# Kernel optimization log

Hardware: AMD Instinct MI355X
Metric: run time of the kernel (lower is better)

Reference implementation:

```python
import jax, jax.numpy as jnp
import numpy as np

N, E = 50000, 400000
N_INP, H, D = 256, 4, 32
HID = H * D
TN, TE, L, N_OUT = 4, 6, 2, 16
SQRT_D = float(np.sqrt(D))


def setup_inputs() -> dict:
    key = jax.random.key(0)
    ks = jax.random.split(key, 16)
    s = 0.05
    return {
        "x": jax.random.normal(ks[0], (N, N_INP), jnp.float32),
        "adapt_W": jax.random.normal(ks[1], (TN, N_INP, HID), jnp.float32) * s,
        "adapt_b": jnp.zeros((TN, HID), jnp.float32),
        "Wk": jax.random.normal(ks[2], (L, TN, HID, HID), jnp.float32) * s,
        "Wq": jax.random.normal(ks[3], (L, TN, HID, HID), jnp.float32) * s,
        "Wv": jax.random.normal(ks[4], (L, TN, HID, HID), jnp.float32) * s,
        "pri": jnp.ones((L, H, TE), jnp.float32),
        "Wa": jax.random.normal(ks[5], (L, H, TE, D, D), jnp.float32) * s,
        "Wm": jax.random.normal(ks[6], (L, H, TE, D, D), jnp.float32) * s,
        "Wla": jax.random.normal(ks[7], (L, TN, HID, HID), jnp.float32) * s,
        "skip": jnp.ones((L, TN), jnp.float32),
        "gamma": jnp.ones((L, HID), jnp.float32),
        "beta": jnp.zeros((L, HID), jnp.float32),
        "out_W": jax.random.normal(ks[8], (HID, N_OUT), jnp.float32) * s,
        "out_b": jnp.zeros((N_OUT,), jnp.float32),
        "ntype": jax.random.randint(ks[9], (N,), 0, TN),
        "etype": jax.random.randint(ks[10], (E,), 0, TE),
        "src": jax.random.randint(ks[11], (E,), 0, N),
        "dst": jax.random.randint(ks[12], (E,), 0, N),
    }


def typed_linear(x, W, types):
    # out[i] = x[i] @ W[types[i]]  (TypedLinear / per-type nn.Linear loop)
    out = jnp.zeros((x.shape[0], W.shape[-1]), x.dtype)
    for t in range(W.shape[0]):
        out = jnp.where((types == t)[:, None], x @ W[t], out)
    return out


def hgt_layer(h, ntype, etype, src, dst, Wk, Wq, Wv, pri, Wa, Wm, Wla, skip, gamma, beta):
    k = typed_linear(h, Wk, ntype).reshape(N, H, D)
    q = typed_linear(h, Wq, ntype).reshape(N, H, D)
    v = typed_linear(h, Wv, ntype).reshape(N, H, D)
    k_e, q_e, v_e = k[src], q[dst], v[src]  # [E,H,D] gathers
    a = jnp.zeros((E, H), h.dtype)
    m = jnp.zeros((E, H, D), h.dtype)
    for t in range(TE):  # small fixed loop over edge types (relation matrices)
        sel = etype == t
        kw = jnp.einsum('ehd,hdo->eho', k_e, Wa[:, t])
        sc = (kw * q_e).sum(-1) * pri[:, t][None, :] / SQRT_D  # [E,H]
        a = jnp.where(sel[:, None], sc, a)
        mt = jnp.einsum('ehd,hdo->eho', v_e, Wm[:, t])
        m = jnp.where(sel[:, None, None], mt, m)
    # edge softmax over incoming edges of each destination node
    amax = jax.ops.segment_max(a, dst, num_segments=N)
    ex = jnp.exp(a - amax[dst])
    den = jax.ops.segment_sum(ex, dst, num_segments=N)
    attn = ex / den[dst]
    agg = jax.ops.segment_sum(m * attn[:, :, None], dst, num_segments=N).reshape(N, HID)
    ha = typed_linear(agg, Wla, ntype)
    alpha = jax.nn.sigmoid(skip)[ntype][:, None]
    out = ha * alpha + h * (1.0 - alpha)
    mu = out.mean(-1, keepdims=True)
    var = jnp.mean((out - mu) ** 2, -1, keepdims=True)
    return (out - mu) / jnp.sqrt(var + 1e-5) * gamma + beta


def forward(x, adapt_W, adapt_b, Wk, Wq, Wv, pri, Wa, Wm, Wla, skip, gamma, beta, out_W, out_b, ntype, etype, src, dst):
    # per-node-type adapt linear + exact GELU
    h = typed_linear(x, adapt_W, ntype) + adapt_b[ntype]
    h = jax.nn.gelu(h, approximate=False)
    for l in range(L):
        h = hgt_layer(h, ntype, etype, src, dst, Wk[l], Wq[l], Wv[l], pri[l], Wa[l], Wm[l], Wla[l], skip[l], gamma[l], beta[l])
    return h @ out_W + out_b


def reference(x, adapt_W, adapt_b, Wk, Wq, Wv, pri, Wa, Wm, Wla, skip, gamma, beta, out_W, out_b, ntype, etype, src, dst):
    return forward(x, adapt_W, adapt_b, Wk, Wq, Wv, pri, Wa, Wm, Wla, skip, gamma, beta, out_W, out_b, ntype, etype, src, dst)
```

## Files before the change

### kernel.cpp

```cpp
#include <hip/hip_runtime.h>
#include <hip/hip_bf16.h>
#include <math.h>

#define NN   50000
#define EE   400000
#define NINP 256
#define HH   4
#define DD   32
#define HIDD 128
#define TNN  4
#define TEE  6
#define LLL  2
#define NOUTT 16
#define NB   196


typedef __attribute__((ext_vector_type(8))) short bf16x8;
typedef __attribute__((ext_vector_type(4))) float f32x4;

__device__ __forceinline__ float bf_lo(unsigned u) { return __uint_as_float(u << 16); }
__device__ __forceinline__ float bf_hi(unsigned u) { return __uint_as_float(u & 0xFFFF0000u); }
__device__ __forceinline__ unsigned f2bf(float f) {
    unsigned u = __float_as_uint(f);
    u += 0x7FFFu + ((u >> 16) & 1u);
    return (u >> 16);
}

__global__ void k_init(int* __restrict__ deg, int* __restrict__ cur, int* __restrict__ ncnt,
                       int* __restrict__ ncur, int* __restrict__ nperm) {
    int i = blockIdx.x * 256 + threadIdx.x;
    if (i < NN) { deg[i] = 0; cur[i] = 0; }
    if (i < 16) { ncnt[i] = 0; ncur[i] = 0; }
    if (i < NN + 512) nperm[i] = -1;
}

__global__ void k_count_edges(const int* __restrict__ dst, int* __restrict__ deg) {
    int e = blockIdx.x * 256 + threadIdx.x;
    if (e < EE) atomicAdd(&deg[dst[e]], 1);
}
__global__ void k_count_types(const int* __restrict__ ntype, int* __restrict__ ncnt) {
    int n = blockIdx.x * 256 + threadIdx.x;
    int lane = threadIdx.x & 63;
    int t = (n < NN) ? ntype[n] : -1;
#pragma unroll
    for (int tt = 0; tt < TNN; tt++) {
        unsigned long long mask = __ballot(t == tt);
        if (mask && lane == (__ffsll((unsigned long long)mask) - 1))
            atomicAdd(&ncnt[tt], __popcll(mask));
    }
}
__global__ void k_scan1(const int* __restrict__ deg, int* __restrict__ bsum) {
    int i = blockIdx.x * 256 + threadIdx.x;
    int lane = threadIdx.x & 63, wv = threadIdx.x >> 6;
    __shared__ int ws[4];
    int x = (i < NN) ? deg[i] : 0;
#pragma unroll
    for (int off = 1; off < 64; off <<= 1) x += __shfl_xor(x, off);
    if (lane == 0) ws[wv] = x;
    __syncthreads();
    if (threadIdx.x == 0) bsum[blockIdx.x] = ws[0] + ws[1] + ws[2] + ws[3];
}
__global__ void k_scan2(const int* __restrict__ bsum, int* __restrict__ bpre,
                        const int* __restrict__ ncnt, int* __restrict__ meta) {
    __shared__ int ws[4];
    int tid = threadIdx.x, lane = tid & 63, wv = tid >> 6;
    int v = (tid < NB) ? bsum[tid] : 0;
    int x = v;
#pragma unroll
    for (int off = 1; off < 64; off <<= 1) {
        int y = __shfl_up(x, off);
        if (lane >= off) x += y;
    }
    if (lane == 63) ws[wv] = x;
    __syncthreads();
    if (tid == 0) { int a = 0; for (int w = 0; w < 4; w++) { int s = ws[w]; ws[w] = a; a += s; } }
    __syncthreads();
    if (tid < NB) bpre[tid] = x - v + ws[wv];
    if (tid == 0) {
        int acc = 0;
        meta[0] = 0;
        for (int t = 0; t < TNN; t++) { acc += ((ncnt[t] + 63) >> 6) << 6; meta[t + 1] = acc; }
    }
}
__global__ void k_scan3(const int* __restrict__ deg, const int* __restrict__ bpre,
                        int* __restrict__ offs) {
    int b = blockIdx.x;
    int tid = threadIdx.x, lane = tid & 63, wv = tid >> 6;
    int i = b * 256 + tid;
    __shared__ int ws[4];
    int v = (i < NN) ? deg[i] : 0;
    int x = v;
#pragma unroll
    for (int off = 1; off < 64; off <<= 1) {
        int y = __shfl_up(x, off);
        if (lane >= off) x += y;
    }
    if (lane == 63) ws[wv] = x;
    __syncthreads();
    if (tid == 0) { int a = 0; for (int w = 0; w < 4; w++) { int s = ws[w]; ws[w] = a; a += s; } }
    __syncthreads();
    if (i < NN) offs[i + 1] = x + ws[wv] + bpre[b];
    if (b == 0 && tid == 0) offs[0] = 0;
}
__global__ void k_scatter_edges(const int* __restrict__ dst, const int* __restrict__ offs,
                                int* __restrict__ cur, int* __restrict__ eidx) {
    int e = blockIdx.x * 256 + threadIdx.x;
    if (e < EE) {
        int d = dst[e];
        int p = atomicAdd(&cur[d], 1);
        eidx[offs[d] + p] = e;
    }
}
__global__ void k_scatter_nodes(const int* __restrict__ ntype, const int* __restrict__ meta,
                                int* __restrict__ ncur, int* __restrict__ nperm) {
    int n = blockIdx.x * 256 + threadIdx.x;
    int lane = threadIdx.x & 63;
    int t = (n < NN) ? ntype[n] : -1;
#pragma unroll
    for (int tt = 0; tt < TNN; tt++) {
        unsigned long long mask = __ballot(t == tt);
        if (t == tt) {
            int rank = __popcll(mask & ((1ull << lane) - 1ull));
            int leader = __ffsll((unsigned long long)mask) - 1;
            int b = 0;
            if (rank == 0) b = atomicAdd(&ncur[tt], __popcll(mask));
            b = __shfl(b, leader);
            nperm[meta[tt] + b + rank] = n;
        }
    }
}

__global__ void k_wt(const float* __restrict__ adapt_W, const float* __restrict__ Wk,
                     const float* __restrict__ Wla, unsigned short* __restrict__ adaptT,
                     unsigned short* __restrict__ Wf, unsigned short* __restrict__ WlaT) {
    __shared__ float Ts[64][68];
    int b = blockIdx.x, tid = threadIdx.x;
    const float* src;
    unsigned short* dst;
    int K, kt, nt;
    if (b < 32) {
        int t = b >> 3, tile = b & 7;
        K = 256; kt = tile >> 1; nt = tile & 1;
        src = adapt_W + (size_t)t * 256 * 128;
        dst = adaptT + (size_t)t * 128 * 256;
    } else if (b < 64) {
        int b2 = b - 32, l = b2 >> 4, r = b2 & 15, t = r >> 2, tile = r & 3;
        K = 128; kt = tile >> 1; nt = tile & 1;
        src = Wk + (size_t)(l * 4 + t) * 16384;
        dst = Wf + (size_t)(l * TNN + t) * 1664 * 128;
    } else {
        int b2 = b - 64, l = b2 >> 4, r = b2 & 15, t = r >> 2, tile = r & 3;
        K = 128; kt = tile >> 1; nt = tile & 1;
        src = Wla + (size_t)(l * 4 + t) * 16384;
        dst = WlaT + (size_t)(l * 4 + t) * 16384;
    }
    int k0 = kt * 64, n0 = nt * 64;
#pragma unroll
    for (int it = 0; it < 4; it++) {
        int idx = tid + it * 256;
        int row = idx >> 4, c4 = (idx & 15) * 4;
        *(float4*)(&Ts[row][c4]) = *(const float4*)(src + (size_t)(k0 + row) * 128 + n0 + c4);
    }
    __syncthreads();
#pragma unroll
    for (int it = 0; it < 2; it++) {
        int idx = tid + it * 256;
        int nn = idx >> 3, sg = (idx & 7) * 8;
        uint4 pk;
        pk.x = f2bf(Ts[sg + 0][nn]) | (f2bf(Ts[sg + 1][nn]) << 16);
        pk.y = f2bf(Ts[sg + 2][nn]) | (f2bf(Ts[sg + 3][nn]) << 16);
        pk.z = f2bf(Ts[sg + 4][nn]) | (f2bf(Ts[sg + 5][nn]) << 16);
        pk.w = f2bf(Ts[sg + 6][nn]) | (f2bf(Ts[sg + 7][nn]) << 16);
        *(uint4*)(dst + (size_t)(n0 + nn) * K + k0 + sg) = pk;
    }
}

__global__ void k_comb(const float* __restrict__ Wq, const float* __restrict__ Wa,
                       const float* __restrict__ Wv, const float* __restrict__ Wm,
                       const float* __restrict__ pri, unsigned short* __restrict__ Wf) {
    __shared__ float Ls[128][36];
    __shared__ float Ss[32][36];
    __shared__ unsigned short Ot[32][136];
    int b = blockIdx.x, tid = threadIdx.x;
    int mode = b / 192;
    int rem = b % 192;
    int l = rem / 96;
    int rem2 = rem % 96;
    int t = rem2 / 24;
    int ht = rem2 % 24;
    int hh = ht / 6, te = ht % 6;
    const float* L = (mode == 0 ? Wq : Wv) + ((size_t)(l * TNN + t)) * 16384;
    const float* S = (mode == 0 ? Wa : Wm) + ((size_t)((l * HH + hh) * TEE + te)) * 1024;
    float ps = (mode == 0) ? pri[(l * HH + hh) * TEE + te] * 0.17677669529663687f : 1.0f;
#pragma unroll
    for (int it = 0; it < 4; it++) {
        int idx = tid + it * 256;
        int kk = idx >> 3, c4 = (idx & 7) * 4;
        *(float4*)(&Ls[kk][c4]) = *(const float4*)(L + (size_t)kk * 128 + hh * 32 + c4);
    }
    {
        int r = tid >> 3, c4 = (tid & 7) * 4;
        *(float4*)(&Ss[r][c4]) = *(const float4*)(S + r * 32 + c4);
    }
    __syncthreads();
    int k = tid >> 1, half = tid & 1;
#pragma unroll
    for (int jj = 0; jj < 16; jj++) {
        int j = half * 16 + jj;
        float s = 0.f;
        if (mode == 0) {
#pragma unroll
            for (int o = 0; o < 32; o++) s += Ls[k][o] * Ss[j][o];
        } else {
#pragma unroll
            for (int d = 0; d < 32; d++) s += Ls[k][d] * Ss[d][j];
        }
        Ot[j][k] = (unsigned short)f2bf(s * ps);
    }
    __syncthreads();
    unsigned short* dst = Wf + ((size_t)(l * TNN + t) * 1664 + (mode == 0 ? 128 : 896)) * 128;
#pragma unroll
    for (int it = 0; it < 2; it++) {
        int idx = tid + it * 256;
        int j = idx >> 4, sg = (idx & 15) * 8;
        uint4 pk = *(const uint4*)(&Ot[j][sg]);
        int jg = (hh * 6 + te) * 32 + j;
        *(uint4*)(dst + (size_t)jg * 128 + sg) = pk;
    }
}

template <int K, int NCB, int EPI, int OMODE, int AF32>
__launch_bounds__(256) __global__
void k_gemm(const void* __restrict__ Av, const unsigned short* __restrict__ WT,
            const float* __restrict__ bias, float* __restrict__ Yf,
            unsigned short* __restrict__ Yb, const int* __restrict__ nperm,
            const int* __restrict__ meta, const float* __restrict__ skipv,
            const float* __restrict__ gamma, const float* __restrict__ beta,
            float* __restrict__ hres, unsigned short* __restrict__ hbout) {
    __shared__ __align__(16) char smem[52224];
    unsigned short* Ab = (unsigned short*)smem;
    unsigned short* Bs = (unsigned short*)(smem + 17408);
    float* Cb = (float*)(smem + 17408);
    const int WIDTH = NCB * 128;
    int row0 = blockIdx.x * 64;
    if (row0 >= meta[4]) return;
    int t = 0;
    while (t < 3 && row0 >= meta[t + 1]) t++;
    const unsigned short* WTt = WT + (size_t)t * WIDTH * K;
    int tid = threadIdx.x;
    int lane = tid & 63, w = tid >> 6;
    int m = lane & 15, q = lane >> 4;

#pragma unroll 1
    for (int cb = 0; cb < NCB; cb++) {
        f32x4 acc[8];
#pragma unroll
        for (int g = 0; g < 8; g++) acc[g] = (f32x4){0.f, 0.f, 0.f, 0.f};
#pragma unroll
        for (int kc = 0; kc < K / 128; kc++) {
            __syncthreads();
            if (NCB == 1 || cb == 0) {
                if (AF32) {
                    const float* A = (const float*)Av;
#pragma unroll
                    for (int it = 0; it < 8; it++) {
                        int idx = tid + it * 256;
                        int r = idx >> 5, c4 = (idx & 31) * 4;
                        int node = nperm[row0 + r];
                        float4 v = make_float4(0.f, 0.f, 0.f, 0.f);
                        if (node >= 0)
                            v = *(const float4*)(A + (size_t)node * K + kc * 128 + c4);
                        uint2 pk;
                        pk.x = f2bf(v.x) | (f2bf(v.y) << 16);
                        pk.y = f2bf(v.z) | (f2bf(v.w) << 16);
                        *(uint2*)(Ab + r * 136 + c4) = pk;
                    }
                } else {
                    const unsigned short* A = (const unsigned short*)Av;
#pragma unroll
                    for (int it = 0; it < 4; it++) {
                        int idx = tid + it * 256;
                        int r = idx >> 4, sg = idx & 15;
                        int node = nperm[row0 + r];
                        uint4 v = make_uint4(0, 0, 0, 0);
                        if (node >= 0)
                            v = *(const uint4*)(A + (size_t)node * K + kc * 128 + sg * 8);
                        *(uint4*)(Ab + r * 136 + sg * 8) = v;
                    }
                }
            }
#pragma unroll
            for (int it = 0; it < 8; it++) {
                int idx = tid + it * 256;
                int n = idx >> 4, sg = idx & 15;
                *(uint4*)(Bs + n * 136 + sg * 8) =
                    *(const uint4*)(WTt + (size_t)(cb * 128 + n) * K + kc * 128 + sg * 8);
            }
            __syncthreads();
#pragma unroll
            for (int k0 = 0; k0 < 128; k0 += 32) {
                bf16x8 a = *(const bf16x8*)(Ab + (w * 16 + m) * 136 + k0 + q * 8);
#pragma unroll
                for (int g = 0; g < 8; g++) {
                    bf16x8 bb = *(const bf16x8*)(Bs + (g * 16 + m) * 136 + k0 + q * 8);
                    acc[g] = __builtin_amdgcn_mfma_f32_16x16x32_bf16(a, bb, acc[g], 0, 0, 0);
                }
            }
        }
        __syncthreads();
#pragma unroll
        for (int g = 0; g < 8; g++)
#pragma unroll
            for (int r = 0; r < 4; r++)
                Cb[(w * 16 + q * 4 + r) * 132 + g * 16 + m] = acc[g][r];
        __syncthreads();
        if (EPI == 2) {
            float alpha = 1.0f / (1.0f + __expf(-skipv[t]));
            int off = lane * 2;
            float2 g2 = *(const float2*)(gamma + off);
            float2 b2 = *(const float2*)(beta + off);
#pragma unroll 1
            for (int it = 0; it < 16; it++) {
                int row = w * 16 + it;
                int node = nperm[row0 + row];
                if (node < 0) continue;
                float ax = Cb[row * 132 + off];
                float ay = Cb[row * 132 + off + 1];
                float2 h2 = *(const float2*)(hres + (size_t)node * 128 + off);
                float ox = ax * alpha + h2.x * (1.f - alpha);
                float oy = ay * alpha + h2.y * (1.f - alpha);
                float s = ox + oy;
#pragma unroll
                for (int mm = 1; mm < 64; mm <<= 1) s += __shfl_xor(s, mm);
                float mu = s * (1.0f / 128.0f);
                float dx = ox - mu, dy = oy - mu;
                float v2 = dx * dx + dy * dy;
#pragma unroll
                for (int mm = 1; mm < 64; mm <<= 1) v2 += __shfl_xor(v2, mm);
                float rs = rsqrtf(v2 * (1.0f / 128.0f) + 1e-5f);
                float vx = dx * rs * g2.x + b2.x;
                float vy = dy * rs * g2.y + b2.y;
                *(float2*)(hres + (size_t)node * 128 + off) = make_float2(vx, vy);
                *(unsigned*)(hbout + (size_t)node * 128 + off) = f2bf(vx) | (f2bf(vy) << 16);
            }
        } else {
#pragma unroll
            for (int it = 0; it < 8; it++) {
                int idx = tid + it * 256;
                int row = idx >> 5, c4 = (idx & 31) * 4;
                int node = nperm[row0 + row];
                if (node < 0) continue;
                float4 v = *(const float4*)(Cb + row * 132 + c4);
                if (EPI == 1) {
                    float4 bv = *(const float4*)(bias + t * 128 + c4);
                    v.x += bv.x; v.y += bv.y; v.z += bv.z; v.w += bv.w;
                    const float is2 = 0.70710678118654752f;
                    v.x = 0.5f * v.x * (1.f + erff(v.x * is2));
                    v.y = 0.5f * v.y * (1.f + erff(v.y * is2));
                    v.z = 0.5f * v.z * (1.f + erff(v.z * is2));
                    v.w = 0.5f * v.w * (1.f + erff(v.w * is2));
                }
                int col = cb * 128 + c4;
                if (OMODE == 0 || OMODE == 2)
                    *(float4*)(Yf + (size_t)node * WIDTH + col) = v;
                if (OMODE == 1 || OMODE == 2) {
                    uint2 pk;
                    pk.x = f2bf(v.x) | (f2bf(v.y) << 16);
                    pk.y = f2bf(v.z) | (f2bf(v.w) << 16);
                    *(uint2*)(Yb + (size_t)node * WIDTH + col) = pk;
                }
            }
        }
    }
}

__global__ void k_edge(const unsigned short* __restrict__ kqv,
                       const int* __restrict__ offs, const int* __restrict__ eidx,
                       const int* __restrict__ src, const int* __restrict__ etype,
                       unsigned short* __restrict__ aggb) {
    int lane = threadIdx.x & 63;
    int wid = blockIdx.x * (blockDim.x >> 6) + (threadIdx.x >> 6);
    int nw = gridDim.x * (blockDim.x >> 6);
    int h = lane >> 4;
    int i2 = (lane & 15) * 2;
    int hoff = h * 32 + i2;
    for (int n = wid; n < NN; n += nw) {
        int e0 = offs[n], e1 = offs[n + 1];
        float ax = 0.f, ay = 0.f, den = 0.f;
        const unsigned short* qrow = kqv + (size_t)n * 1664 + 128;
        int s[4], t[4];
#pragma unroll
        for (int u = 0; u < 4; u++) {
            s[u] = 0; t[u] = 0;
            if (e0 + u < e1) { int e = eidx[e0 + u]; s[u] = src[e]; t[u] = etype[e]; }
        }
        int j = e0;
        while (j + 3 < e1) {
            unsigned ku[4], qu[4], vu[4];
#pragma unroll
            for (int u = 0; u < 4; u++) {
                int to = (h * 6 + t[u]) * 32 + i2;
                ku[u] = *(const unsigned*)(kqv + (size_t)s[u] * 1664 + hoff);
                qu[u] = *(const unsigned*)(qrow + to);
                vu[u] = *(const unsigned*)(kqv + (size_t)s[u] * 1664 + 896 + to);
            }
            int jn = j + 4;
#pragma unroll
            for (int u = 0; u < 4; u++)
                if (jn + u < e1) { int e = eidx[jn + u]; s[u] = src[e]; t[u] = etype[e]; }
            float p[4];
#pragma unroll
            for (int u = 0; u < 4; u++)
                p[u] = bf_lo(ku[u]) * bf_lo(qu[u]) + bf_hi(ku[u]) * bf_hi(qu[u]);
#pragma unroll
            for (int mm = 1; mm < 16; mm <<= 1) {
#pragma unroll
                for (int u = 0; u < 4; u++) p[u] += __shfl_xor(p[u], mm);
            }
#pragma unroll
            for (int u = 0; u < 4; u++) {
                float ex = __expf(p[u]);
                den += ex;
                ax += ex * bf_lo(vu[u]);
                ay += ex * bf_hi(vu[u]);
            }
            j = jn;
        }
        for (int u = 0; j < e1; j++, u++) {
            int to = (h * 6 + t[u]) * 32 + i2;
            unsigned ku = *(const unsigned*)(kqv + (size_t)s[u] * 1664 + hoff);
            unsigned qu = *(const unsigned*)(qrow + to);
            unsigned vu = *(const unsigned*)(kqv + (size_t)s[u] * 1664 + 896 + to);
            float p0 = bf_lo(ku) * bf_lo(qu) + bf_hi(ku) * bf_hi(qu);
            p0 += __shfl_xor(p0, 1);
            p0 += __shfl_xor(p0, 2);
            p0 += __shfl_xor(p0, 4);
            p0 += __shfl_xor(p0, 8);
            float ex = __expf(p0);
            den += ex;
            ax += ex * bf_lo(vu);
            ay += ex * bf_hi(vu);
        }
        float r = (den > 0.f) ? (1.0f / den) : 0.f;
        unsigned pk = f2bf(ax * r) | (f2bf(ay * r) << 16);
        *(unsigned*)(aggb + (size_t)n * 128 + hoff) = pk;
    }
}

__global__ void k_out(const unsigned short* __restrict__ hb, const float* __restrict__ Wo,
                      const float* __restrict__ bo, float* __restrict__ out) {
    __shared__ float Ws[128 * 16];
    int tid = threadIdx.x;
#pragma unroll
    for (int it = 0; it < 2; it++) {
        int idx = (tid + it * 256) * 4;
        *(float4*)(&Ws[idx]) = *(const float4*)(Wo + idx);
    }
    __syncthreads();
    int nl = tid >> 4;
    int o = tid & 15;
    int n = blockIdx.x * 16 + nl;
    float acc = bo[o];
    const unsigned short* hr = hb + (size_t)n * 128;
#pragma unroll
    for (int kk = 0; kk < 128; kk += 8) {
        uint4 hv = *(const uint4*)(hr + kk);
        acc += bf_lo(hv.x) * Ws[(kk + 0) * 16 + o] + bf_hi(hv.x) * Ws[(kk + 1) * 16 + o] +
               bf_lo(hv.y) * Ws[(kk + 2) * 16 + o] + bf_hi(hv.y) * Ws[(kk + 3) * 16 + o] +
               bf_lo(hv.z) * Ws[(kk + 4) * 16 + o] + bf_hi(hv.z) * Ws[(kk + 5) * 16 + o] +
               bf_lo(hv.w) * Ws[(kk + 6) * 16 + o] + bf_hi(hv.w) * Ws[(kk + 7) * 16 + o];
    }
    out[(size_t)n * 16 + o] = acc;
}

extern "C" void kernel_launch(void* const* d_in, const int* in_sizes, int n_in,
                              void* d_out, int out_size, void* d_ws, size_t ws_size,
                              hipStream_t stream) {
    const float* x       = (const float*)d_in[0];
    const float* adapt_W = (const float*)d_in[1];
    const float* adapt_b = (const float*)d_in[2];
    const float* Wk      = (const float*)d_in[3];
    const float* Wq      = (const float*)d_in[4];
    const float* Wv      = (const float*)d_in[5];
    const float* pri     = (const float*)d_in[6];
    const float* Wa      = (const float*)d_in[7];
    const float* Wm      = (const float*)d_in[8];
    const float* Wla     = (const float*)d_in[9];
    const float* skip    = (const float*)d_in[10];
    const float* gamma   = (const float*)d_in[11];
    const float* beta    = (const float*)d_in[12];
    const float* out_W   = (const float*)d_in[13];
    const float* out_b   = (const float*)d_in[14];
    const int* ntype     = (const int*)d_in[15];
    const int* etype     = (const int*)d_in[16];
    const int* src       = (const int*)d_in[17];
    const int* dst       = (const int*)d_in[18];
    float* out = (float*)d_out;

    char* p = (char*)d_ws;
    auto al = [](size_t v) { return (v + 255) & ~(size_t)255; };
    float* h  = (float*)p;          p += al((size_t)NN * 128 * 4);
    unsigned short* hb   = (unsigned short*)p; p += al((size_t)NN * 128 * 2);
    unsigned short* aggb = (unsigned short*)p; p += al((size_t)NN * 128 * 2);
    unsigned short* kqvb = (unsigned short*)p; p += al((size_t)NN * 1664 * 2);
    unsigned short* adaptT = (unsigned short*)p; p += al((size_t)TNN * 128 * 256 * 2);
    unsigned short* WlaT   = (unsigned short*)p; p += al((size_t)LLL * TNN * 16384 * 2);
    unsigned short* Wf     = (unsigned short*)p; p += al((size_t)LLL * TNN * 1664 * 128 * 2);
    int* deg   = (int*)p; p += al((size_t)NN * 4);
    int* offs  = (int*)p; p += al((size_t)(NN + 1) * 4);
    int* cur   = (int*)p; p += al((size_t)NN * 4);
    int* eidx  = (int*)p; p += al((size_t)EE * 4);
    int* nperm = (int*)p; p += al((size_t)(NN + 512) * 4);
    int* bsum  = (int*)p; p += al(256 * 4);
    int* bpre  = (int*)p; p += al(256 * 4);
    int* ncnt  = (int*)p; p += al(64);
    int* ncur  = (int*)p; p += al(64);
    int* meta  = (int*)p; p += al(64);

    k_init<<<(NN + 512 + 255) / 256, 256, 0, stream>>>(deg, cur, ncnt, ncur, nperm);
    k_count_edges<<<(EE + 255) / 256, 256, 0, stream>>>(dst, deg);
    k_count_types<<<(NN + 255) / 256, 256, 0, stream>>>(ntype, ncnt);
    k_scan1<<<NB, 256, 0, stream>>>(deg, bsum);
    k_scan2<<<1, 256, 0, stream>>>(bsum, bpre, ncnt, meta);
    k_scan3<<<NB, 256, 0, stream>>>(deg, bpre, offs);
    k_scatter_edges<<<(EE + 255) / 256, 256, 0, stream>>>(dst, offs, cur, eidx);
    k_scatter_nodes<<<(NN + 255) / 256, 256, 0, stream>>>(ntype, meta, ncur, nperm);

    k_wt<<<96, 256, 0, stream>>>(adapt_W, Wk, Wla, adaptT, Wf, WlaT);
    k_comb<<<384, 256, 0, stream>>>(Wq, Wa, Wv, Wm, pri, Wf);

    const int TILES = NN / 64 + TNN + 1;

    k_gemm<256, 1, 1, 2, 1><<<TILES, 256, 0, stream>>>(
        x, adaptT, adapt_b, h, hb, nperm, meta, nullptr, nullptr, nullptr, nullptr, nullptr);

    for (int l = 0; l < LLL; l++) {
        k_gemm<128, 13, 0, 1, 0><<<TILES, 256, 0, stream>>>(
            hb, Wf + (size_t)l * TNN * 1664 * 128, nullptr, nullptr, kqvb, nperm, meta,
            nullptr, nullptr, nullptr, nullptr, nullptr);

        k_edge<<<4096, 256, 0, stream>>>(kqvb, offs, eidx, src, etype, aggb);

        k_gemm<128, 1, 2, 0, 0><<<TILES, 256, 0, stream>>>(
            aggb, WlaT + (size_t)l * TNN * 16384, nullptr, nullptr, nullptr, nperm, meta,
            skip + (size_t)l * TNN, gamma + (size_t)l * HIDD, beta + (size_t)l * HIDD,
            h, hb);
    }

    k_out<<<NN / 16, 256, 0, stream>>>(hb, out_W, out_b, out);
}
```

Before: 681.7 us.

## Pack src/etype into CSR edge list and stream GEMM weights from global

The edge scatter now stores a packed word holding (src<<3)|etype per CSR slot, so the edge kernel reads one array instead of an index plus two indirect gathers. The typed GEMM no longer stages the weight tile in shared memory. MFMA B fragments are loaded straight from global/L2, which removes the per-chunk B copy and one barrier, and for the 13-block KQV GEMM the A tile is loaded only once. The epilogue for non-layernorm modes writes accumulators out in two 64-column halves through a smaller shared buffer. This cuts LDS use and may raise occupancy, at the cost of repeated uncoalesced global reads of weights inside the inner MFMA loop.

New measurement: 935.9 us. +37.3%, slower.

```diff
diff --git a/kernel.cpp b/kernel.cpp
--- a/kernel.cpp
+++ b/kernel.cpp
@@ -102,13 +102,14 @@
     if (i < NN) offs[i + 1] = x + ws[wv] + bpre[b];
     if (b == 0 && tid == 0) offs[0] = 0;
 }
-__global__ void k_scatter_edges(const int* __restrict__ dst, const int* __restrict__ offs,
-                                int* __restrict__ cur, int* __restrict__ eidx) {
+__global__ void k_scatter_edges(const int* __restrict__ dst, const int* __restrict__ src,
+                                const int* __restrict__ etype, const int* __restrict__ offs,
+                                int* __restrict__ cur, unsigned* __restrict__ se) {
     int e = blockIdx.x * 256 + threadIdx.x;
     if (e < EE) {
         int d = dst[e];
         int p = atomicAdd(&cur[d], 1);
-        eidx[offs[d] + p] = e;
+        se[offs[d] + p] = ((unsigned)src[e] << 3) | (unsigned)etype[e];
     }
 }
 __global__ void k_scatter_nodes(const int* __restrict__ ntype, const int* __restrict__ meta,
@@ -237,10 +238,9 @@
             const int* __restrict__ meta, const float* __restrict__ skipv,
             const float* __restrict__ gamma, const float* __restrict__ beta,
             float* __restrict__ hres, unsigned short* __restrict__ hbout) {
-    __shared__ __align__(16) char smem[52224];
-    unsigned short* Ab = (unsigned short*)smem;
-    unsigned short* Bs = (unsigned short*)(smem + 17408);
-    float* Cb = (float*)(smem + 17408);
+    constexpr int CBS = (EPI == 2) ? 132 : 68;
+    __shared__ __align__(16) unsigned short Ab[64 * 136];
+    __shared__ __align__(16) float Cb[64 * CBS];
     const int WIDTH = NCB * 128;
     int row0 = blockIdx.x * 64;
     if (row0 >= meta[4]) return;
@@ -258,8 +258,8 @@
         for (int g = 0; g < 8; g++) acc[g] = (f32x4){0.f, 0.f, 0.f, 0.f};
 #pragma unroll
         for (int kc = 0; kc < K / 128; kc++) {
-            __syncthreads();
             if (NCB == 1 || cb == 0) {
+                __syncthreads();
                 if (AF32) {
                     const float* A = (const float*)Av;
 #pragma unroll
@@ -288,33 +288,27 @@
                         *(uint4*)(Ab + r * 136 + sg * 8) = v;
                     }
                 }
-            }
-#pragma unroll
-            for (int it = 0; it < 8; it++) {
-                int idx = tid + it * 256;
-                int n = idx >> 4, sg = idx & 15;
-                *(uint4*)(Bs + n * 136 + sg * 8) =
-                    *(const uint4*)(WTt + (size_t)(cb * 128 + n) * K + kc * 128 + sg * 8);
-            }
-            __syncthreads();
+                __syncthreads();
+            }
+            const unsigned short* Bbase = WTt + (size_t)cb * 128 * K + (size_t)kc * 128;
 #pragma unroll
             for (int k0 = 0; k0 < 128; k0 += 32) {
                 bf16x8 a = *(const bf16x8*)(Ab + (w * 16 + m) * 136 + k0 + q * 8);
 #pragma unroll
                 for (int g = 0; g < 8; g++) {
-                    bf16x8 bb = *(const bf16x8*)(Bs + (g * 16 + m) * 136 + k0 + q * 8);
+                    bf16x8 bb = *(const bf16x8*)(Bbase + (size_t)(g * 16 + m) * K + k0 + q * 8);
                     acc[g] = __builtin_amdgcn_mfma_f32_16x16x32_bf16(a, bb, acc[g], 0, 0, 0);
                 }
             }
         }
-        __syncthreads();
-#pragma unroll
-        for (int g = 0; g < 8; g++)
-#pragma unroll
-            for (int r = 0; r < 4; r++)
-                Cb[(w * 16 + q * 4 + r) * 132 + g * 16 + m] = acc[g][r];
-        __syncthreads();
         if (EPI == 2) {
+            __syncthreads();
+#pragma unroll
+            for (int g = 0; g < 8; g++)
+#pragma unroll
+                for (int r = 0; r < 4; r++)
+                    Cb[(w * 16 + q * 4 + r) * 132 + g * 16 + m] = acc[g][r];
+            __syncthreads();
             float alpha = 1.0f / (1.0f + __expf(-skipv[t]));
             int off = lane * 2;
             float2 g2 = *(const float2*)(gamma + off);
@@ -344,39 +338,48 @@
                 *(unsigned*)(hbout + (size_t)node * 128 + off) = f2bf(vx) | (f2bf(vy) << 16);
             }
         } else {
-#pragma unroll
-            for (int it = 0; it < 8; it++) {
-                int idx = tid + it * 256;
-                int row = idx >> 5, c4 = (idx & 31) * 4;
-                int node = nperm[row0 + row];
-                if (node < 0) continue;
-                float4 v = *(const float4*)(Cb + row * 132 + c4);
-                if (EPI == 1) {
-                    float4 bv = *(const float4*)(bias + t * 128 + c4);
-                    v.x += bv.x; v.y += bv.y; v.z += bv.z; v.w += bv.w;
-                    const float is2 = 0.70710678118654752f;
-                    v.x = 0.5f * v.x * (1.f + erff(v.x * is2));
-                    v.y = 0.5f * v.y * (1.f + erff(v.y * is2));
-                    v.z = 0.5f * v.z * (1.f + erff(v.z * is2));
-                    v.w = 0.5f * v.w * (1.f + erff(v.w * is2));
+#pragma unroll 1
+            for (int hf = 0; hf < 2; hf++) {
+                __syncthreads();
+#pragma unroll
+                for (int g = 0; g < 4; g++)
+#pragma unroll
+                    for (int r = 0; r < 4; r++)
+                        Cb[(w * 16 + q * 4 + r) * 68 + g * 16 + m] = acc[hf * 4 + g][r];
+                __syncthreads();
+#pragma unroll
+                for (int it = 0; it < 4; it++) {
+                    int idx = tid + it * 256;
+                    int row = idx >> 4, c4 = (idx & 15) * 4;
+                    int node = nperm[row0 + row];
+                    if (node < 0) continue;
+                    float4 v = *(const float4*)(Cb + row * 68 + c4);
+                    if (EPI == 1) {
+                        float4 bv = *(const float4*)(bias + t * 128 + hf * 64 + c4);
+                        v.x += bv.x; v.y += bv.y; v.z += bv.z; v.w += bv.w;
+                        const float is2 = 0.70710678118654752f;
+                        v.x = 0.5f * v.x * (1.f + erff(v.x * is2));
+                        v.y = 0.5f * v.y * (1.f + erff(v.y * is2));
+                        v.z = 0.5f * v.z * (1.f + erff(v.z * is2));
+                        v.w = 0.5f * v.w * (1.f + erff(v.w * is2));
+                    }
+                    int col = cb * 128 + hf * 64 + c4;
+                    if (OMODE == 0 || OMODE == 2)
+                        *(float4*)(Yf + (size_t)node * WIDTH + col) = v;
+                    if (OMODE == 1 || OMODE == 2) {
+                        uint2 pk;
+                        pk.x = f2bf(v.x) | (f2bf(v.y) << 16);
+                        pk.y = f2bf(v.z) | (f2bf(v.w) << 16);
+                        *(uint2*)(Yb + (size_t)node * WIDTH + col) = pk;
+                    }
                 }
-                int col = cb * 128 + c4;
-                if (OMODE == 0 || OMODE == 2)
-                    *(float4*)(Yf + (size_t)node * WIDTH + col) = v;
-                if (OMODE == 1 || OMODE == 2) {
-                    uint2 pk;
-                    pk.x = f2bf(v.x) | (f2bf(v.y) << 16);
-                    pk.y = f2bf(v.z) | (f2bf(v.w) << 16);
-                    *(uint2*)(Yb + (size_t)node * WIDTH + col) = pk;
-                }
             }
         }
     }
 }
 
 __global__ void k_edge(const unsigned short* __restrict__ kqv,
-                       const int* __restrict__ offs, const int* __restrict__ eidx,
-                       const int* __restrict__ src, const int* __restrict__ etype,
+                       const int* __restrict__ offs, const unsigned* __restrict__ se,
                        unsigned short* __restrict__ aggb) {
     int lane = threadIdx.x & 63;
     int wid = blockIdx.x * (blockDim.x >> 6) + (threadIdx.x >> 6);
@@ -392,7 +395,7 @@
 #pragma unroll
         for (int u = 0; u < 4; u++) {
             s[u] = 0; t[u] = 0;
-            if (e0 + u < e1) { int e = eidx[e0 + u]; s[u] = src[e]; t[u] = etype[e]; }
+            if (e0 + u < e1) { unsigned p0 = se[e0 + u]; s[u] = p0 >> 3; t[u] = p0 & 7; }
         }
         int j = e0;
         while (j + 3 < e1) {
@@ -407,7 +410,7 @@
             int jn = j + 4;
 #pragma unroll
             for (int u = 0; u < 4; u++)
-                if (jn + u < e1) { int e = eidx[jn + u]; s[u] = src[e]; t[u] = etype[e]; }
+                if (jn + u < e1) { unsigned p0 = se[jn + u]; s[u] = p0 >> 3; t[u] = p0 & 7; }
             float p[4];
 #pragma unroll
             for (int u = 0; u < 4; u++)
@@ -509,7 +512,7 @@
     int* deg   = (int*)p; p += al((size_t)NN * 4);
     int* offs  = (int*)p; p += al((size_t)(NN + 1) * 4);
     int* cur   = (int*)p; p += al((size_t)NN * 4);
-    int* eidx  = (int*)p; p += al((size_t)EE * 4);
+    unsigned* se = (unsigned*)p; p += al((size_t)EE * 4);
     int* nperm = (int*)p; p += al((size_t)(NN + 512) * 4);
     int* bsum  = (int*)p; p += al(256 * 4);
     int* bpre  = (int*)p; p += al(256 * 4);
@@ -523,7 +526,7 @@
     k_scan1<<<NB, 256, 0, stream>>>(deg, bsum);
     k_scan2<<<1, 256, 0, stream>>>(bsum, bpre, ncnt, meta);
     k_scan3<<<NB, 256, 0, stream>>>(deg, bpre, offs);
-    k_scatter_edges<<<(EE + 255) / 256, 256, 0, stream>>>(dst, offs, cur, eidx);
+    k_scatter_edges<<<(EE + 255) / 256, 256, 0, stream>>>(dst, src, etype, offs, cur, se);
     k_scatter_nodes<<<(NN + 255) / 256, 256, 0, stream>>>(ntype, meta, ncur, nperm);
 
     k_wt<<<96, 256, 0, stream>>>(adapt_W, Wk, Wla, adaptT, Wf, WlaT);
@@ -539,7 +542,7 @@
             hb, Wf + (size_t)l * TNN * 1664 * 128, nullptr, nullptr, kqvb, nperm, meta,
             nullptr, nullptr, nullptr, nullptr, nullptr);
 
-        k_edge<<<4096, 256, 0, stream>>>(kqvb, offs, eidx, src, etype, aggb);
+        k_edge<<<4096, 256, 0, stream>>>(kqvb, offs, se, aggb);
 
         k_gemm<128, 1, 2, 0, 0><<<TILES, 256, 0, stream>>>(
             aggb, WlaT + (size_t)l * TNN * 16384, nullptr, nullptr, nullptr, nperm, meta,
```
